# Kernel tuning notes

Hardware: AMD Instinct MI355X
Metric: run time of the kernel (lower is better)

The kernel has to match this reference:

```python
import jax, jax.numpy as jnp
import numpy as np

B, N, T, E = 8, 4096, 16, 65536
D, H, O = 768, 4, 256
PER_TURN = N // T
NEG = -1e30


def setup_inputs() -> dict:
    key = jax.random.key(0)
    k = jax.random.split(key, 10)
    x = jax.random.normal(k[0], (B, N, D), dtype=jnp.float32)
    # turns sorted within each graph: node i has turn i // PER_TURN
    turns = jnp.tile(jnp.repeat(jnp.arange(T, dtype=jnp.int32), PER_TURN)[None, :], (B, 1))
    # edges: dst uniform over nodes, src uniform over nodes with turn[src] <= turn[dst]
    dst = jax.random.randint(k[1], (B, E), 0, N, dtype=jnp.int32)
    bound = (dst // PER_TURN + 1) * PER_TURN
    u = jax.random.uniform(k[2], (B, E), dtype=jnp.float32)
    src = jnp.minimum((u * bound).astype(jnp.int32), bound - 1)
    edge_index = jnp.stack([src, dst], axis=1)  # [B, 2, E]
    W = jax.random.normal(k[3], (D, H * D), dtype=jnp.float32) * 0.02
    a_src = jax.random.normal(k[4], (H, D), dtype=jnp.float32) * 0.05
    a_dst = jax.random.normal(k[5], (H, D), dtype=jnp.float32) * 0.05
    b_gat = jnp.zeros((D,), jnp.float32)
    w_att = jax.random.normal(k[6], (D, 1), dtype=jnp.float32) * 0.05
    b_att = jnp.zeros((1,), jnp.float32)
    w_cls = jax.random.normal(k[7], (D, O), dtype=jnp.float32) * 0.05
    b_cls = jnp.zeros((O,), jnp.float32)
    return dict(x=x, edge_index=edge_index, turns=turns, W=W, a_src=a_src,
                a_dst=a_dst, b_gat=b_gat, w_att=w_att, b_att=b_att,
                w_cls=w_cls, b_cls=b_cls)


def _forward(x, edge_index, turns, W, a_src, a_dst, b_gat, w_att, b_att, w_cls, b_cls, n_turns):
    n = x.shape[1]
    h_heads, d = a_src.shape

    def graph_fn(args):
        xg, ei, tg = args
        src, dst = ei[0], ei[1]

        def step(xc, t):
            active = tg <= t                                  # subgraph node mask [N]
            h = (xc @ W).reshape(n, h_heads, d)               # [N,H,D] per-head projections
            asrc = jnp.einsum('nhd,hd->nh', h, a_src)         # [N,H]
            adst = jnp.einsum('nhd,hd->nh', h, a_dst)
            emask = tg[dst] == t                              # only edges into current turn
            e = jax.nn.leaky_relu(asrc[src] + adst[dst], 0.2)  # [E,H]
            e = jnp.where(emask[:, None], e, NEG)
            # PyG GATConv add_self_loops=True: self-loop on every subgraph node
            s = jax.nn.leaky_relu(asrc + adst, 0.2)           # [N,H]
            s = jnp.where(active[:, None], s, NEG)
            m = jnp.maximum(jax.ops.segment_max(e, dst, num_segments=n), s)
            m = jnp.where(m > NEG * 0.5, m, 0.0)              # safe max for empty segments
            ee = jnp.where(emask[:, None], jnp.exp(e - m[dst]), 0.0)   # [E,H]
            se = jnp.where(active[:, None], jnp.exp(s - m), 0.0)       # [N,H]
            denom = jax.ops.segment_sum(ee, dst, num_segments=n) + se  # [N,H]
            msg = jax.ops.segment_sum(ee[:, :, None] * h[src], dst, num_segments=n)
            out = (msg + se[:, :, None] * h) / jnp.where(denom > 0, denom, 1.0)[:, :, None]
            out = out.mean(axis=1) + b_gat                    # concat=False -> mean over heads
            xn = jnp.where(active[:, None], out, xc)          # write back into graph.x
            # GlobalAttention pooling over subgraph nodes
            gate = (xn @ w_att + b_att).squeeze(-1)           # [N]
            g = jax.nn.softmax(jnp.where(active, gate, NEG))
            pooled = g @ xn                                   # [D]
            return xn, pooled @ w_cls + b_cls                 # [O]

        _, outs = jax.lax.scan(step, xg, jnp.arange(n_turns))
        return outs                                           # [T,O]

    outs = jax.lax.map(graph_fn, (x, edge_index, turns))      # sequential over graphs
    return outs[:, :, None, :]                                # [B,T,1,O] like torch.stack nesting


def reference(x, edge_index, turns, W, a_src, a_dst, b_gat, w_att, b_att, w_cls, b_cls):
    n_turns = int(turns.max()) + 1
    return _forward(x, edge_index, turns, W, a_src, a_dst, b_gat, w_att, b_att,
                    w_cls, b_cls, n_turns)
```

## Files before the change

kernel.cpp:

```cpp
#include <hip/hip_runtime.h>

typedef __attribute__((ext_vector_type(8))) short short8;
typedef __attribute__((ext_vector_type(8))) unsigned short ushort8;
typedef __attribute__((ext_vector_type(4))) float f32x4;

__device__ __forceinline__ float b2f(unsigned short u){
  union { unsigned int i; float f; } v; v.i = ((unsigned int)u)<<16; return v.f;
}
__device__ __forceinline__ unsigned short f2b(float f){
  unsigned int x = __float_as_uint(f);
  return (unsigned short)((x + 0x7fffu + ((x>>16)&1u))>>16);
}

__device__ __forceinline__ void gload16(const unsigned short* g, unsigned short* l){
  __builtin_amdgcn_global_load_lds((const __attribute__((address_space(1))) unsigned int*)g,
                                   (__attribute__((address_space(3))) unsigned int*)l, 16, 0, 0);
}

__global__ __launch_bounds__(256) void k_zero(int* p){
  p[blockIdx.x*256 + threadIdx.x] = 0;
}

__global__ __launch_bounds__(256) void k_hist(const int* __restrict__ ei, int* __restrict__ cnt){
  int idx = blockIdx.x*256 + threadIdx.x;
  int b = idx>>16, e = idx&65535;
  int dst = ei[b*131072 + 65536 + e];
  atomicAdd(&cnt[b*4096 + dst], 1);
}

__global__ __launch_bounds__(1024) void k_scan(int* __restrict__ cnt, int* __restrict__ offs){
  int b = blockIdx.x, tid = threadIdx.x;
  __shared__ int sums[1024];
  int base = tid*4;
  int c0 = cnt[b*4096+base+0], c1 = cnt[b*4096+base+1];
  int c2 = cnt[b*4096+base+2], c3 = cnt[b*4096+base+3];
  int t1 = c0, t2 = c0+c1, t3 = c0+c1+c2, tot = t3+c3;
  sums[tid] = tot;
  __syncthreads();
  for (int off=1; off<1024; off<<=1){
    int add = (tid>=off) ? sums[tid-off] : 0;
    __syncthreads();
    sums[tid] += add;
    __syncthreads();
  }
  int eb = sums[tid] - tot;
  offs[b*4097+base+0] = eb;      offs[b*4097+base+1] = eb+t1;
  offs[b*4097+base+2] = eb+t2;   offs[b*4097+base+3] = eb+t3;
  cnt[b*4096+base+0] = eb;       cnt[b*4096+base+1] = eb+t1;
  cnt[b*4096+base+2] = eb+t2;    cnt[b*4096+base+3] = eb+t3;
  if (tid==1023) offs[b*4097+4096] = sums[1023];
}

__global__ __launch_bounds__(256) void k_scatter(const int* __restrict__ ei, int* __restrict__ cur,
                                                 int* __restrict__ ss){
  int idx = blockIdx.x*256 + threadIdx.x;
  int b = idx>>16, e = idx&65535;
  int src = ei[b*131072 + e];
  int dst = ei[b*131072 + 65536 + e];
  int pos = atomicAdd(&cur[b*4096 + dst], 1);
  ss[b*65536 + pos] = src;
}

__global__ __launch_bounds__(256) void k_vavd(const float* __restrict__ W, const float* __restrict__ a_src,
                                              const float* __restrict__ a_dst, float* __restrict__ vavd){
  int wid = blockIdx.x*4 + (threadIdx.x>>6);
  int lane = threadIdx.x & 63;
  int i = wid>>3, h8 = wid&7, h = h8&3;
  const float* a = (h8<4 ? a_src : a_dst) + h*768;
  const float* wrow = W + i*3072 + h*768;
  float acc = 0.f;
  #pragma unroll
  for (int j12=0; j12<12; j12++){ int j = lane + j12*64; acc += wrow[j]*a[j]; }
  #pragma unroll
  for (int d=1; d<64; d<<=1) acc += __shfl_xor(acc, d);
  if (lane==0) vavd[i*8 + h8] = acc;
}

__global__ __launch_bounds__(256) void k_prep_w(const float* __restrict__ W, unsigned short* __restrict__ wmT,
                                                unsigned short* __restrict__ wpT){
  int g = blockIdx.x*256 + threadIdx.x;
  int i = g%768, j = g/768;
  float s = 0.f;
  #pragma unroll
  for (int h=0; h<4; h++){
    float w = W[i*3072 + h*768 + j];
    s += w;
    wpT[j*3072 + h*768 + i] = f2b(w);
  }
  wmT[j*768 + i] = f2b(0.25f*s);
}

__global__ __launch_bounds__(256) void k_prep0(const float* __restrict__ x0, const float* __restrict__ vavd,
                                               float* __restrict__ ad0, unsigned short* __restrict__ x0b){
  int b = blockIdx.y;
  int node = blockIdx.x*4 + (threadIdx.x>>6);
  int lane = threadIdx.x & 63;
  size_t roff = (size_t)(b*4096 + node)*768;
  float acc[8];
  #pragma unroll
  for (int k=0;k<8;k++) acc[k]=0.f;
  #pragma unroll
  for (int j12=0; j12<12; j12++){
    int j = lane + j12*64;
    float xv = x0[roff + j];
    x0b[roff + j] = f2b(xv);
    const float* vp = vavd + j*8;
    #pragma unroll
    for (int k=0;k<8;k++) acc[k]+=xv*vp[k];
  }
  #pragma unroll
  for (int k=0;k<8;k++){
    #pragma unroll
    for (int d=1; d<64; d<<=1) acc[k] += __shfl_xor(acc[k], d);
  }
  if (lane==0){
    float* o = ad0 + (size_t)(b*4096 + node)*8;
    #pragma unroll
    for (int k=0;k<8;k++) o[k]=acc[k];
  }
}

__global__ __launch_bounds__(256) void k_edge(const unsigned short* __restrict__ x0b, const unsigned short* __restrict__ stc,
                                              const float* __restrict__ ad, const float* __restrict__ ad0,
                                              const int* __restrict__ offs,
                                              const int* __restrict__ ssrc, unsigned short* __restrict__ zbuf, int t){
  int b = blockIdx.y, dl = blockIdx.x, tid = threadIdx.x;
  int dst = t*256 + dl;
  int lane = tid&63, wv = tid>>6;
  int e0 = offs[b*4097 + dst], e1 = offs[b*4097 + dst + 1];
  const float* adr = ad0 + (size_t)(b*4096 + dst)*8;
  float ad0_=adr[4], ad1_=adr[5], ad2_=adr[6], ad3_=adr[7];
  float sh[4];
  { float v;
    v=adr[0]+ad0_; sh[0]=v>0.f?v:0.2f*v;
    v=adr[1]+ad1_; sh[1]=v>0.f?v:0.2f*v;
    v=adr[2]+ad2_; sh[2]=v>0.f?v:0.2f*v;
    v=adr[3]+ad3_; sh[3]=v>0.f?v:0.2f*v; }
  int band = t*256;
  float mx[4] = {-1e30f,-1e30f,-1e30f,-1e30f};
  for (int i=e0+tid; i<e1; i+=256){
    int s = ssrc[b*65536 + i];
    const float* ap = (s >= band ? ad0 : ad) + (size_t)(b*4096 + s)*8;
    float v;
    v=ap[0]+ad0_; v=v>0.f?v:0.2f*v; mx[0]=fmaxf(mx[0],v);
    v=ap[1]+ad1_; v=v>0.f?v:0.2f*v; mx[1]=fmaxf(mx[1],v);
    v=ap[2]+ad2_; v=v>0.f?v:0.2f*v; mx[2]=fmaxf(mx[2],v);
    v=ap[3]+ad3_; v=v>0.f?v:0.2f*v; mx[3]=fmaxf(mx[3],v);
  }
  #pragma unroll
  for (int h=0;h<4;h++){
    #pragma unroll
    for (int d=1; d<64; d<<=1) mx[h] = fmaxf(mx[h], __shfl_xor(mx[h], d));
  }
  __shared__ float redm[4][4];
  if (lane==0){ redm[wv][0]=mx[0]; redm[wv][1]=mx[1]; redm[wv][2]=mx[2]; redm[wv][3]=mx[3]; }
  __syncthreads();
  float m[4];
  #pragma unroll
  for (int h=0;h<4;h++)
    m[h] = fmaxf(fmaxf(fmaxf(redm[0][h],redm[1][h]),fmaxf(redm[2][h],redm[3][h])), sh[h]);

  __shared__ float4 eeL[256];
  __shared__ int srcL[256];
  float den0=0.f,den1=0.f,den2=0.f,den3=0.f;
  float za[4][3] = {{0,0,0},{0,0,0},{0,0,0},{0,0,0}};
  for (int base=e0; base<e1; base+=256){
    __syncthreads();
    int i = base + tid;
    if (i < e1){
      int s = ssrc[b*65536 + i];
      const float* ap = (s >= band ? ad0 : ad) + (size_t)(b*4096 + s)*8;
      float4 wq; float v;
      v=ap[0]+ad0_; v=v>0.f?v:0.2f*v; wq.x=expf(v-m[0]); den0+=wq.x;
      v=ap[1]+ad1_; v=v>0.f?v:0.2f*v; wq.y=expf(v-m[1]); den1+=wq.y;
      v=ap[2]+ad2_; v=v>0.f?v:0.2f*v; wq.z=expf(v-m[2]); den2+=wq.z;
      v=ap[3]+ad3_; v=v>0.f?v:0.2f*v; wq.w=expf(v-m[3]); den3+=wq.w;
      eeL[tid] = wq; srcL[tid] = s;
    }
    __syncthreads();
    int cnt = e1 - base; if (cnt > 256) cnt = 256;
    for (int k=0; k<cnt; k++){
      float4 wq = eeL[k];
      int s = srcL[k];
      const unsigned short* r = (s < band ? stc : x0b) + (size_t)(b*4096 + s)*768;
      float xv0=b2f(r[tid]), xv1=b2f(r[tid+256]), xv2=b2f(r[tid+512]);
      za[0][0]+=wq.x*xv0; za[0][1]+=wq.x*xv1; za[0][2]+=wq.x*xv2;
      za[1][0]+=wq.y*xv0; za[1][1]+=wq.y*xv1; za[1][2]+=wq.y*xv2;
      za[2][0]+=wq.z*xv0; za[2][1]+=wq.z*xv1; za[2][2]+=wq.z*xv2;
      za[3][0]+=wq.w*xv0; za[3][1]+=wq.w*xv1; za[3][2]+=wq.w*xv2;
    }
  }
  float se[4];
  #pragma unroll
  for (int h=0;h<4;h++) se[h] = expf(sh[h]-m[h]);
  { const unsigned short* r = x0b + (size_t)(b*4096 + dst)*768;
    float xv0=b2f(r[tid]), xv1=b2f(r[tid+256]), xv2=b2f(r[tid+512]);
    za[0][0]+=se[0]*xv0; za[0][1]+=se[0]*xv1; za[0][2]+=se[0]*xv2;
    za[1][0]+=se[1]*xv0; za[1][1]+=se[1]*xv1; za[1][2]+=se[1]*xv2;
    za[2][0]+=se[2]*xv0; za[2][1]+=se[2]*xv1; za[2][2]+=se[2]*xv2;
    za[3][0]+=se[3]*xv0; za[3][1]+=se[3]*xv1; za[3][2]+=se[3]*xv2; }
  float den[4]={den0,den1,den2,den3};
  #pragma unroll
  for (int h=0;h<4;h++){
    #pragma unroll
    for (int d=1; d<64; d<<=1) den[h] += __shfl_xor(den[h], d);
  }
  __shared__ float redd[4][4];
  if (lane==0){ redd[wv][0]=den[0]; redd[wv][1]=den[1]; redd[wv][2]=den[2]; redd[wv][3]=den[3]; }
  __syncthreads();
  unsigned short* zp = zbuf + (size_t)(b*256 + dl)*3072;
  #pragma unroll
  for (int h=0;h<4;h++){
    float dtot = redd[0][h]+redd[1][h]+redd[2][h]+redd[3][h] + se[h];
    float sc = 0.25f/dtot;
    zp[h*768 + tid      ] = f2b(za[h][0]*sc);
    zp[h*768 + tid + 256] = f2b(za[h][1]*sc);
    zp[h*768 + tid + 512] = f2b(za[h][2]*sc);
  }
}

__global__ __launch_bounds__(512) void k_mm(const unsigned short* __restrict__ zbuf,
                                            const unsigned short* __restrict__ wpT,
                                            const unsigned short* __restrict__ stc,
                                            const unsigned short* __restrict__ wmT,
                                            const float* __restrict__ bias,
                                            unsigned short* __restrict__ partA,
                                            unsigned short* __restrict__ stn, int t){
  int nwg = gridDim.x, orig = blockIdx.x;
  int cpx = nwg>>3;
  int j = (orig&7)*cpx + (orig>>3);

  int tid = threadIdx.x, lane = tid&63, w = tid>>6;
  bool jobA = j < 192;
  const unsigned short *Ap, *Bp;
  int lda, ldb, s = 0, b = 0, mrow, ncol;
  if (jobA){
    s = j/48; int q = j%48;
    mrow = (q/6)*256; ncol = (q%6)*128;
    Ap = zbuf + (size_t)mrow*3072 + s*768;  lda = 3072;
    Bp = wpT  + (size_t)ncol*3072 + s*768;  ldb = 3072;
  } else {
    int idx = j - 192; int pg = 6*t;
    b = idx/pg; int rr = idx%pg;
    mrow = (rr/6)*256; ncol = (rr%6)*128;
    Ap = stc + (size_t)b*4096*768 + (size_t)mrow*768;  lda = 768;
    Bp = wmT + (size_t)ncol*768;                       ldb = 768;
  }
  int wr = (w>>1)*64, wc = (w&1)*64;
  int lrow = lane&15, lk = (lane>>4)*8;
  __shared__ unsigned short As[3][256*32];
  __shared__ unsigned short Bs[3][128*32];
  f32x4 acc[4][4];
  #pragma unroll
  for (int m=0;m<4;m++)
    #pragma unroll
    for (int n2=0;n2<4;n2++) acc[m][n2] = (f32x4){0.f,0.f,0.f,0.f};
  int srow = w*16 + (lane>>2);
  int skb  = (lane&3)*8;
  const unsigned short* ga0 = Ap + (size_t)srow*lda + skb;
  const unsigned short* ga1 = Ap + (size_t)(128+srow)*lda + skb;
  const unsigned short* gb0 = Bp + (size_t)srow*ldb + skb;
  int lo = w*512;
  #define STAGE(bi) { gload16(ga0, &As[bi][lo]); gload16(ga1, &As[bi][4096+lo]); \
                      gload16(gb0, &Bs[bi][lo]); \
                      ga0 += 32; ga1 += 32; gb0 += 32; }
  STAGE(0)
  STAGE(1)
  #pragma unroll
  for (int kt=0; kt<24; kt++){
    int cur = kt%3;
    if (kt < 22) STAGE((kt+2)%3)
    if (kt < 22)      asm volatile("s_waitcnt vmcnt(6)" ::: "memory");
    else if (kt==22)  asm volatile("s_waitcnt vmcnt(3)" ::: "memory");
    else              asm volatile("s_waitcnt vmcnt(0)" ::: "memory");
    __builtin_amdgcn_sched_barrier(0);
    __builtin_amdgcn_s_barrier();
    __builtin_amdgcn_sched_barrier(0);
    short8 af[4], bf[4];
    #pragma unroll
    for (int m=0;m<4;m++)  af[m]  = *(const short8*)&As[cur][(wr + m*16 + lrow)*32 + lk];
    #pragma unroll
    for (int n2=0;n2<4;n2++) bf[n2] = *(const short8*)&Bs[cur][(wc + n2*16 + lrow)*32 + lk];
    __builtin_amdgcn_s_setprio(1);
    #pragma unroll
    for (int m=0;m<4;m++)
      #pragma unroll
      for (int n2=0;n2<4;n2++)
        acc[m][n2] = __builtin_amdgcn_mfma_f32_16x16x32_bf16(af[m], bf[n2], acc[m][n2], 0,0,0);
    __builtin_amdgcn_s_setprio(0);
    __builtin_amdgcn_sched_barrier(0);
    __builtin_amdgcn_s_barrier();
    __builtin_amdgcn_sched_barrier(0);
  }
  #undef STAGE
  if (jobA){
    unsigned short* op = partA + (size_t)s*2048*768;
    #pragma unroll
    for (int m=0;m<4;m++)
      #pragma unroll
      for (int n2=0;n2<4;n2++)
        #pragma unroll
        for (int r=0;r<4;r++){
          int gr = mrow + wr + m*16 + (lane>>4)*4 + r;
          int gc = ncol + wc + n2*16 + (lane&15);
          op[(size_t)gr*768 + gc] = f2b(acc[m][n2][r]);
        }
  } else {
    unsigned short* cp = stn + (size_t)b*4096*768;
    #pragma unroll
    for (int m=0;m<4;m++)
      #pragma unroll
      for (int n2=0;n2<4;n2++)
        #pragma unroll
        for (int r=0;r<4;r++){
          int gr = mrow + wr + m*16 + (lane>>4)*4 + r;
          int gc = ncol + wc + n2*16 + (lane&15);
          cp[(size_t)gr*768 + gc] = f2b(acc[m][n2][r] + bias[gc]);
        }
  }
}

__global__ __launch_bounds__(256) void k_post(const unsigned short* __restrict__ partA, const float* __restrict__ bias,
                                              const float* __restrict__ vavd, const float* __restrict__ w_att,
                                              const unsigned short* __restrict__ st,
                                              unsigned short* __restrict__ stn, float* __restrict__ ad,
                                              float* __restrict__ gate, int t){
  int j = blockIdx.x, tid = threadIdx.x;
  int lane = tid&63, wv = tid>>6;
  if (j < 2048){
    int r = j;
    int g = r>>8;
    size_t e = (size_t)r*768;
    const size_t SL = (size_t)2048*768;
    int c0 = tid, c1 = tid+256, c2 = tid+512;
    float v0 = b2f(partA[e+c0]) + b2f(partA[SL+e+c0]) + b2f(partA[2*SL+e+c0]) + b2f(partA[3*SL+e+c0]) + bias[c0];
    float v1 = b2f(partA[e+c1]) + b2f(partA[SL+e+c1]) + b2f(partA[2*SL+e+c1]) + b2f(partA[3*SL+e+c1]) + bias[c1];
    float v2 = b2f(partA[e+c2]) + b2f(partA[SL+e+c2]) + b2f(partA[2*SL+e+c2]) + b2f(partA[3*SL+e+c2]) + bias[c2];
    size_t ro = ((size_t)g*4096 + t*256 + (r&255))*768;
    stn[ro+c0] = f2b(v0); stn[ro+c1] = f2b(v1); stn[ro+c2] = f2b(v2);
    float acc[9];
    const float *p0 = vavd + c0*8, *p1 = vavd + c1*8, *p2 = vavd + c2*8;
    #pragma unroll
    for (int k=0;k<8;k++) acc[k] = v0*p0[k] + v1*p1[k] + v2*p2[k];
    acc[8] = v0*w_att[c0] + v1*w_att[c1] + v2*w_att[c2];
    #pragma unroll
    for (int k=0;k<9;k++){
      #pragma unroll
      for (int d=1; d<64; d<<=1) acc[k] += __shfl_xor(acc[k], d);
    }
    __shared__ float red[4][9];
    if (lane==0){
      #pragma unroll
      for (int k=0;k<9;k++) red[wv][k]=acc[k];
    }
    __syncthreads();
    if (tid==0){
      size_t no = (size_t)g*4096 + t*256 + (r&255);
      float* o = ad + no*8;
      #pragma unroll
      for (int k=0;k<8;k++) o[k] = red[0][k]+red[1][k]+red[2][k]+red[3][k];
      gate[no] = red[0][8]+red[1][8]+red[2][8]+red[3][8];
    }
  } else {
    int idx = j - 2048;
    int per = t*64;
    int b = idx/per;
    int node = (idx%per)*4 + (tid>>6);
    size_t roff = (size_t)(b*4096 + node)*768;
    float acc[9];
    #pragma unroll
    for (int k=0;k<9;k++) acc[k]=0.f;
    #pragma unroll
    for (int j12=0; j12<12; j12++){
      int jj = lane + j12*64;
      float xv = b2f(st[roff + jj]);
      const float* vp = vavd + jj*8;
      acc[0]+=xv*vp[0]; acc[1]+=xv*vp[1]; acc[2]+=xv*vp[2]; acc[3]+=xv*vp[3];
      acc[4]+=xv*vp[4]; acc[5]+=xv*vp[5]; acc[6]+=xv*vp[6]; acc[7]+=xv*vp[7];
      acc[8]+=xv*w_att[jj];
    }
    #pragma unroll
    for (int k=0;k<9;k++){
      #pragma unroll
      for (int d=1; d<64; d<<=1) acc[k] += __shfl_xor(acc[k], d);
    }
    if (lane==0){
      float* o = ad + (size_t)(b*4096 + node)*8;
      #pragma unroll
      for (int k=0;k<8;k++) o[k]=acc[k];
      gate[b*4096 + node] = acc[8];
    }
  }
}

__global__ __launch_bounds__(256) void k_pool(const unsigned short* __restrict__ st, const float* __restrict__ gate,
                                              float* __restrict__ part, int t){
  int b = blockIdx.y, bx = blockIdx.x, tid = threadIdx.x;
  int lane = tid&63, wv = tid>>6;
  int A = (t+1)*256;
  const float* g = gate + b*4096;
  float mx = -1e30f;
  for (int i=tid; i<A; i+=256) mx = fmaxf(mx, g[i]);
  #pragma unroll
  for (int d=1; d<64; d<<=1) mx = fmaxf(mx, __shfl_xor(mx, d));
  __shared__ float rm[4];
  if (lane==0) rm[wv]=mx;
  __syncthreads();
  mx = fmaxf(fmaxf(rm[0],rm[1]), fmaxf(rm[2],rm[3]));
  float s = 0.f;
  for (int i=tid; i<A; i+=256) s += expf(g[i]-mx);
  #pragma unroll
  for (int d=1; d<64; d<<=1) s += __shfl_xor(s, d);
  __shared__ float rs[4];
  if (lane==0) rs[wv]=s;
  __syncthreads();
  float invS = 1.f/(rs[0]+rs[1]+rs[2]+rs[3]);
  int slice = A>>5;
  int n0 = bx*slice;
  float a0=0.f, a1=0.f, a2=0.f;
  for (int n=n0; n<n0+slice; n++){
    float wgt = expf(g[n]-mx)*invS;
    const unsigned short* r = st + (size_t)(b*4096 + n)*768;
    a0 += wgt*b2f(r[tid]); a1 += wgt*b2f(r[tid+256]); a2 += wgt*b2f(r[tid+512]);
  }
  float* p = part + (size_t)(b*32 + bx)*768;
  p[tid]=a0; p[tid+256]=a1; p[tid+512]=a2;
}

__global__ __launch_bounds__(256) void k_cls(const float* __restrict__ part, const float* __restrict__ w_cls,
                                             const float* __restrict__ b_cls, float* __restrict__ out, int t){
  int b = blockIdx.x, cg = blockIdx.y, tid = threadIdx.x;
  __shared__ float pooled[768];
  #pragma unroll
  for (int cc=0; cc<3; cc++){
    float s=0.f; int jj = tid + cc*256;
    for (int p=0; p<32; p++) s += part[(size_t)(b*32+p)*768 + jj];
    pooled[jj] = s;
  }
  __syncthreads();
  int col = tid&31, sub = tid>>5;
  int gcol = cg*32 + col;
  float s = 0.f;
  for (int jj=sub*96; jj<sub*96+96; jj++) s += pooled[jj]*w_cls[jj*256 + gcol];
  __shared__ float red[8][32];
  red[sub][col] = s;
  __syncthreads();
  if (tid < 32){
    float acc = b_cls[cg*32+tid];
    #pragma unroll
    for (int k=0;k<8;k++) acc += red[k][tid];
    out[b*4096 + t*256 + cg*32 + tid] = acc;
  }
}

extern "C" void kernel_launch(void* const* d_in, const int* in_sizes, int n_in,
                              void* d_out, int out_size, void* d_ws, size_t ws_size,
                              hipStream_t stream){
  const float* x0    = (const float*)d_in[0];
  const int*   ei    = (const int*)d_in[1];
  const float* W     = (const float*)d_in[3];
  const float* a_src = (const float*)d_in[4];
  const float* a_dst = (const float*)d_in[5];
  const float* b_gat = (const float*)d_in[6];
  const float* w_att = (const float*)d_in[7];
  const float* w_cls = (const float*)d_in[9];
  const float* b_cls = (const float*)d_in[10];
  float* out = (float*)d_out;
  char* ws = (char*)d_ws;

  size_t pos = 0;
  auto alloc = [&](size_t sz)->char*{ char* r = ws + pos; pos = (pos + sz + 255) & ~(size_t)255; return r; };
  unsigned short* st0  = (unsigned short*)alloc((size_t)8*4096*768*2);
  unsigned short* st1  = (unsigned short*)alloc((size_t)8*4096*768*2);
  unsigned short* x0b  = (unsigned short*)alloc((size_t)8*4096*768*2);
  unsigned short* zbuf = (unsigned short*)alloc((size_t)8*256*3072*2);
  float* adbuf = (float*)alloc((size_t)8*4096*8*4);
  float* ad0   = (float*)alloc((size_t)8*4096*8*4);
  float* gate  = (float*)alloc((size_t)8*4096*4);
  int*   ssrc  = (int*)alloc((size_t)8*65536*4);
  int*   offs  = (int*)alloc((size_t)8*4097*4);
  int*   curs  = (int*)alloc((size_t)8*4096*4);
  float* vavd  = (float*)alloc((size_t)768*8*4);
  unsigned short* wm = (unsigned short*)alloc((size_t)768*768*2);
  unsigned short* wp = (unsigned short*)alloc((size_t)768*3072*2);
  float* part  = (float*)alloc((size_t)8*32*768*4);
  unsigned short* partA = (unsigned short*)alloc((size_t)4*2048*768*2);
  unsigned short* st[2] = {st0, st1};

  k_zero   <<<128, 256, 0, stream>>>(curs);
  k_hist   <<<2048, 256, 0, stream>>>(ei, curs);
  k_scan   <<<8, 1024, 0, stream>>>(curs, offs);
  k_scatter<<<2048, 256, 0, stream>>>(ei, curs, ssrc);
  k_vavd   <<<1536, 256, 0, stream>>>(W, a_src, a_dst, vavd);
  k_prep_w <<<2304, 256, 0, stream>>>(W, wm, wp);
  k_prep0  <<<dim3(1024,8), 256, 0, stream>>>(x0, vavd, ad0, x0b);

  for (int t=0; t<16; t++){
    int cur = t&1, nxt = cur^1;
    k_edge<<<dim3(256,8), 256, 0, stream>>>(x0b, st[cur], adbuf, ad0, offs, ssrc, zbuf, t);
    k_mm <<<192 + 48*t, 512, 0, stream>>>(zbuf, wp, st[cur], wm, b_gat, partA, st[nxt], t);
    k_post<<<2048 + t*512, 256, 0, stream>>>(partA, b_gat, vavd, w_att, st[nxt], st[nxt], adbuf, gate, t);
    k_pool<<<dim3(32,8), 256, 0, stream>>>(st[nxt], gate, part, t);
    k_cls <<<dim3(8,8), 256, 0, stream>>>(part, w_cls, b_cls, out, t);
  }
}
```

Baseline: 1.858 ms.

## Fold pooling and classifier into next turn's edge and post kernels

Removes the separate per-turn pool and classifier launches. Attention pooling for turn t-1 now runs as extra blocks inside the next turn's edge kernel, and the classifier for turn t-1 runs as extra blocks inside the next turn's post kernel, with a final pool/cls pair after the loop. This cuts about 30 launches and lets the small tail work overlap with larger kernels. It also vectorises the prep0 loads and stores to float4/ushort4. The cost is more complex indexing, and correctness now depends on the buffer ping-pong still holding the previous turn's state and gate when the fused blocks run.

```diff
diff --git a/kernel.cpp b/kernel.cpp
--- a/kernel.cpp
+++ b/kernel.cpp
@@ -100,13 +100,15 @@
   #pragma unroll
   for (int k=0;k<8;k++) acc[k]=0.f;
   #pragma unroll
-  for (int j12=0; j12<12; j12++){
-    int j = lane + j12*64;
-    float xv = x0[roff + j];
-    x0b[roff + j] = f2b(xv);
-    const float* vp = vavd + j*8;
-    #pragma unroll
-    for (int k=0;k<8;k++) acc[k]+=xv*vp[k];
+  for (int j4=0; j4<3; j4++){
+    int j = j4*256 + lane*4;
+    float4 xv = *(const float4*)&x0[roff + j];
+    ushort4 pk; pk.x=f2b(xv.x); pk.y=f2b(xv.y); pk.z=f2b(xv.z); pk.w=f2b(xv.w);
+    *(ushort4*)&x0b[roff + j] = pk;
+    const float* vp0 = vavd + (size_t)j*8;
+    #pragma unroll
+    for (int k=0;k<8;k++)
+      acc[k] += xv.x*vp0[k] + xv.y*vp0[8+k] + xv.z*vp0[16+k] + xv.w*vp0[24+k];
   }
   #pragma unroll
   for (int k=0;k<8;k++){
@@ -123,10 +125,44 @@
 __global__ __launch_bounds__(256) void k_edge(const unsigned short* __restrict__ x0b, const unsigned short* __restrict__ stc,
                                               const float* __restrict__ ad, const float* __restrict__ ad0,
                                               const int* __restrict__ offs,
-                                              const int* __restrict__ ssrc, unsigned short* __restrict__ zbuf, int t){
-  int b = blockIdx.y, dl = blockIdx.x, tid = threadIdx.x;
+                                              const int* __restrict__ ssrc, unsigned short* __restrict__ zbuf, int t,
+                                              const float* __restrict__ gate, float* __restrict__ part){
+  int bx = blockIdx.x, b = blockIdx.y, tid = threadIdx.x;
+  int lane = tid&63, wv = tid>>6;
+  if (bx >= 256){
+    int slice_i = bx - 256;
+    int A = t*256;
+    const float* g = gate + b*4096;
+    float mx = -1e30f;
+    for (int i=tid; i<A; i+=256) mx = fmaxf(mx, g[i]);
+    #pragma unroll
+    for (int d=1; d<64; d<<=1) mx = fmaxf(mx, __shfl_xor(mx, d));
+    __shared__ float rm[4];
+    if (lane==0) rm[wv]=mx;
+    __syncthreads();
+    mx = fmaxf(fmaxf(rm[0],rm[1]), fmaxf(rm[2],rm[3]));
+    float s = 0.f;
+    for (int i=tid; i<A; i+=256) s += expf(g[i]-mx);
+    #pragma unroll
+    for (int d=1; d<64; d<<=1) s += __shfl_xor(s, d);
+    __shared__ float rs[4];
+    if (lane==0) rs[wv]=s;
+    __syncthreads();
+    float invS = 1.f/(rs[0]+rs[1]+rs[2]+rs[3]);
+    int slice = A>>5;
+    int n0 = slice_i*slice;
+    float a0=0.f, a1=0.f, a2=0.f;
+    for (int n=n0; n<n0+slice; n++){
+      float wgt = expf(g[n]-mx)*invS;
+      const unsigned short* r = stc + (size_t)(b*4096 + n)*768;
+      a0 += wgt*b2f(r[tid]); a1 += wgt*b2f(r[tid+256]); a2 += wgt*b2f(r[tid+512]);
+    }
+    float* p = part + (size_t)(b*32 + slice_i)*768;
+    p[tid]=a0; p[tid+256]=a1; p[tid+512]=a2;
+    return;
+  }
+  int dl = bx;
   int dst = t*256 + dl;
-  int lane = tid&63, wv = tid>>6;
   int e0 = offs[b*4097 + dst], e1 = offs[b*4097 + dst + 1];
   const float* adr = ad0 + (size_t)(b*4096 + dst)*8;
   float ad0_=adr[4], ad1_=adr[5], ad2_=adr[6], ad3_=adr[7];
@@ -324,9 +360,38 @@
                                               const float* __restrict__ vavd, const float* __restrict__ w_att,
                                               const unsigned short* __restrict__ st,
                                               unsigned short* __restrict__ stn, float* __restrict__ ad,
-                                              float* __restrict__ gate, int t){
+                                              float* __restrict__ gate, int t,
+                                              const float* __restrict__ part, const float* __restrict__ w_cls,
+                                              const float* __restrict__ b_cls, float* __restrict__ out){
   int j = blockIdx.x, tid = threadIdx.x;
   int lane = tid&63, wv = tid>>6;
+  int clsbase = 2048 + t*512;
+  if (j >= clsbase){
+    int cidx = j - clsbase;
+    int b = cidx>>3, cg = cidx&7;
+    __shared__ float pooled[768];
+    #pragma unroll
+    for (int cc=0; cc<3; cc++){
+      float ps=0.f; int jj = tid + cc*256;
+      for (int pp=0; pp<32; pp++) ps += part[(size_t)(b*32+pp)*768 + jj];
+      pooled[jj] = ps;
+    }
+    __syncthreads();
+    int col = tid&31, sub = tid>>5;
+    int gcol = cg*32 + col;
+    float s = 0.f;
+    for (int jj=sub*96; jj<sub*96+96; jj++) s += pooled[jj]*w_cls[jj*256 + gcol];
+    __shared__ float red2[8][32];
+    red2[sub][col] = s;
+    __syncthreads();
+    if (tid < 32){
+      float acc2 = b_cls[cg*32+tid];
+      #pragma unroll
+      for (int k=0;k<8;k++) acc2 += red2[k][tid];
+      out[b*4096 + (t-1)*256 + cg*32 + tid] = acc2;
+    }
+    return;
+  }
   if (j < 2048){
     int r = j;
     int g = r>>8;
@@ -497,10 +562,13 @@
 
   for (int t=0; t<16; t++){
     int cur = t&1, nxt = cur^1;
-    k_edge<<<dim3(256,8), 256, 0, stream>>>(x0b, st[cur], adbuf, ad0, offs, ssrc, zbuf, t);
+    int gx = (t==0) ? 256 : 288;
+    k_edge<<<dim3(gx,8), 256, 0, stream>>>(x0b, st[cur], adbuf, ad0, offs, ssrc, zbuf, t, gate, part);
     k_mm <<<192 + 48*t, 512, 0, stream>>>(zbuf, wp, st[cur], wm, b_gat, partA, st[nxt], t);
-    k_post<<<2048 + t*512, 256, 0, stream>>>(partA, b_gat, vavd, w_att, st[nxt], st[nxt], adbuf, gate, t);
-    k_pool<<<dim3(32,8), 256, 0, stream>>>(st[nxt], gate, part, t);
-    k_cls <<<dim3(8,8), 256, 0, stream>>>(part, w_cls, b_cls, out, t);
-  }
-}
+    int px = 2048 + t*512 + ((t>0) ? 64 : 0);
+    k_post<<<px, 256, 0, stream>>>(partA, b_gat, vavd, w_att, st[nxt], st[nxt], adbuf, gate, t,
+                                   part, w_cls, b_cls, out);
+  }
+  k_pool<<<dim3(32,8), 256, 0, stream>>>(st[0], gate, part, 15);
+  k_cls <<<dim3(8,8), 256, 0, stream>>>(part, w_cls, b_cls, out, 15);
+}
```

Measured after the change: 1.754 ms. 5.6% less time.
